# Performance work log

Hardware: AMD Instinct MI355X
Metric: run time of the kernel (lower is better)

Reference implementation:

```python
import jax, jax.numpy as jnp
import numpy as np

G, N, C, R, NCOMP, F = 1, 2097152, 16, 320, 48, 27


def _interp_plane(src, u, v):
    # src: (G, C, H, W). Torch grid_sample convention: u (grid x) indexes W (last dim),
    # v (grid y) indexes H. align_corners=True, bilinear, zero padding. Returns (G, N, C).
    _, _, H, W = src.shape
    x = (u + 1.0) * 0.5 * (W - 1)
    y = (v + 1.0) * 0.5 * (H - 1)
    x0 = jnp.floor(x)
    y0 = jnp.floor(y)
    wx = x - x0
    wy = y - y0
    x0i = x0.astype(jnp.int32)
    y0i = y0.astype(jnp.int32)

    def corner(xi, yi, w):
        inb = ((xi >= 0) & (xi < W) & (yi >= 0) & (yi < H)).astype(src.dtype)
        xc = jnp.clip(xi, 0, W - 1)
        yc = jnp.clip(yi, 0, H - 1)
        vals = jax.vmap(lambda s, yy, xx: s[:, yy, xx])(src, yc, xc)  # (G, C, N)
        return vals * (w * inb)[:, None, :]

    out = (corner(x0i, y0i, (1.0 - wx) * (1.0 - wy))
           + corner(x0i + 1, y0i, wx * (1.0 - wy))
           + corner(x0i, y0i + 1, (1.0 - wx) * wy)
           + corner(x0i + 1, y0i + 1, wx * wy))
    return out.transpose(0, 2, 1)  # (G, N, C)


def _interp_line(src, t):
    # src: (G, C, L), t in [-1, 1]. 1D linear interp, align_corners=True, zero padding.
    _, _, L = src.shape
    x = (t + 1.0) * 0.5 * (L - 1)
    x0 = jnp.floor(x)
    wx = x - x0
    x0i = x0.astype(jnp.int32)

    def corner(xi, w):
        inb = ((xi >= 0) & (xi < L)).astype(src.dtype)
        xc = jnp.clip(xi, 0, L - 1)
        vals = jax.vmap(lambda s, xx: s[:, xx])(src, xc)  # (G, C, N)
        return vals * (w * inb)[:, None, :]

    out = corner(x0i, 1.0 - wx) + corner(x0i + 1, wx)
    return out.transpose(0, 2, 1)  # (G, N, C)


def setup_inputs() -> dict:
    key = jax.random.key(0)
    ks = jax.random.split(key, 8)
    return {
        "points": jax.random.uniform(ks[0], (G, N, 3), jnp.float32, minval=-1.0, maxval=1.0),
        "matrix_components_xy": jax.random.normal(ks[1], (G, C, R, R), jnp.float32) * 0.1,
        "matrix_components_yz": jax.random.normal(ks[2], (G, C, R, R), jnp.float32) * 0.1,
        "matrix_components_xz": jax.random.normal(ks[3], (G, C, R, R), jnp.float32) * 0.1,
        "vector_components_x": jax.random.normal(ks[4], (G, C, R), jnp.float32) * 0.1,
        "vector_components_y": jax.random.normal(ks[5], (G, C, R), jnp.float32) * 0.1,
        "vector_components_z": jax.random.normal(ks[6], (G, C, R), jnp.float32) * 0.1,
        "basis_matrix": jax.random.normal(ks[7], (G, NCOMP, F), jnp.float32) * 0.1,
    }


def reference(points, matrix_components_xy, matrix_components_yz, matrix_components_xz,
              vector_components_x, vector_components_y, vector_components_z, basis_matrix):
    recorded_shape = points.shape
    p = points.reshape(points.shape[0], -1, points.shape[-1])  # (G, N, 3)
    px, py, pz = p[..., 0], p[..., 1], p[..., 2]
    # points[..., :2] -> grid x = px (indexes W of xy plane), grid y = py
    a = _interp_plane(matrix_components_xy, px, py) * _interp_line(vector_components_z, pz)
    # points[..., [0, 2]] -> grid x = px, grid y = pz
    b = _interp_plane(matrix_components_xz, px, pz) * _interp_line(vector_components_y, py)
    # points[..., 1:] -> grid x = py, grid y = pz
    c = _interp_plane(matrix_components_yz, py, pz) * _interp_line(vector_components_x, px)
    feats = jnp.concatenate((a, b, c), axis=-1)  # (G, N, 3C)
    result = jnp.einsum('gnc,gcf->gnf', feats, basis_matrix)  # (G, N, F)
    return result.reshape(*recorded_shape[:-1], -1)
```

## Files before the change

kernel.cpp:

```cpp
#include <hip/hip_runtime.h>
#include <hip/hip_fp16.h>
#include <stdint.h>


constexpr int NPTS = 2097152;
constexpr int CCH  = 16;
constexpr int RES  = 320;
constexpr long long HW = (long long)RES * RES;
constexpr int FD   = 27;
constexpr int BLK  = 256;
constexpr int EBLK = 512;
constexpr int CDIM = 16;
constexpr int NCELL = CDIM * CDIM * CDIM;
constexpr int PATCH = 22;
constexpr int PP_U4 = PATCH * PATCH * 2;
constexpr int PL_U4 = 3 * PP_U4;
constexpr int LN_U4 = 3 * PATCH * 2;
constexpr int SORT_BLOCKS = 256;
constexpr int PTS_PER_SORT = NPTS / SORT_BLOCKS;
constexpr int SORT_G = PTS_PER_SORT / (BLK * 4);

constexpr int PLANE_BLOCKS = 1200;
constexpr int LINE_BLOCKS = 4;

constexpr size_t WS_PLANEH = 0;
constexpr size_t WS_LINEH  = WS_PLANEH + 3ull*HW*CCH*2;
constexpr size_t WS_BFRAG  = WS_LINEH + 3ull*RES*CCH*2;
constexpr size_t WS_CHIST  = WS_BFRAG + 3072;
constexpr size_t WS_CURSOR = WS_CHIST + (size_t)NCELL*4;
constexpr size_t WS_SORTED = WS_CURSOR + (size_t)NCELL*4;
constexpr size_t WS_NEED   = WS_SORTED + (size_t)NPTS*16;

typedef _Float16 half8 __attribute__((ext_vector_type(8)));
typedef float f32x16 __attribute__((ext_vector_type(16)));

__device__ __forceinline__ int cell_key16(float px, float py, float pz) {
    int cx = min(max((int)((px + 1.f) * 8.f), 0), 15);
    int cy = min(max((int)((py + 1.f) * 8.f), 0), 15);
    int cz = min(max((int)((pz + 1.f) * 8.f), 0), 15);
    return (cz << 8) | (cy << 4) | cx;
}

__global__ __launch_bounds__(BLK) void prep_kernel(
    const float* __restrict__ pts,
    const float* __restrict__ pxy, const float* __restrict__ pxz, const float* __restrict__ pyz,
    const float* __restrict__ vx, const float* __restrict__ vy, const float* __restrict__ vz,
    const float* __restrict__ basis,
    __half* __restrict__ planesH, __half* __restrict__ linesH, __half* __restrict__ bfragH,
    unsigned* __restrict__ chist) {
    __shared__ unsigned lh[NCELL];
    const int bid = blockIdx.x;
    const int tid = threadIdx.x;
    if (bid < SORT_BLOCKS) {
        #pragma unroll
        for (int k = 0; k < NCELL / BLK; ++k) lh[tid + k * BLK] = 0u;
        __syncthreads();
        const float4* p4 = ((const float4*)pts) + (size_t)bid * (PTS_PER_SORT * 3 / 4);
        #pragma unroll
        for (int g = 0; g < SORT_G; ++g) {
            const int t = g * BLK + tid;
            const float4 a = p4[t*3+0], b = p4[t*3+1], c = p4[t*3+2];
            atomicAdd(&lh[cell_key16(a.x, a.y, a.z)], 1u);
            atomicAdd(&lh[cell_key16(a.w, b.x, b.y)], 1u);
            atomicAdd(&lh[cell_key16(b.z, b.w, c.x)], 1u);
            atomicAdd(&lh[cell_key16(c.y, c.z, c.w)], 1u);
        }
        __syncthreads();
        #pragma unroll
        for (int k = 0; k < NCELL / BLK; ++k) {
            const int i = tid + k * BLK;
            if (lh[i]) atomicAdd(&chist[i], lh[i]);
        }
    } else if (bid < SORT_BLOCKS + PLANE_BLOCKS) {
        const int pb = bid - SORT_BLOCKS;
        const int plane = pb / 400;
        const int texel = (pb % 400) * BLK + tid;
        const float* src = (plane == 0) ? pxy : (plane == 1 ? pxz : pyz);
        union { ushort u[16]; uint4 q[2]; } pk;
        #pragma unroll
        for (int c = 0; c < CCH; ++c)
            pk.u[c] = __half_as_ushort(__float2half(src[(size_t)c * HW + texel]));
        uint4* dst = (uint4*)(planesH + ((size_t)plane * HW + texel) * CCH);
        dst[0] = pk.q[0]; dst[1] = pk.q[1];
    } else if (bid < SORT_BLOCKS + PLANE_BLOCKS + LINE_BLOCKS) {
        const int idx = (bid - SORT_BLOCKS - PLANE_BLOCKS) * BLK + tid;
        if (idx >= 3 * RES) return;
        const int axis = idx / RES, t = idx % RES;
        const float* src = (axis == 0) ? vx : (axis == 1 ? vy : vz);
        union { ushort u[16]; uint4 q[2]; } pk;
        #pragma unroll
        for (int c = 0; c < CCH; ++c)
            pk.u[c] = __half_as_ushort(__float2half(src[c * RES + t]));
        uint4* dst = (uint4*)(linesH + ((size_t)axis * RES + t) * CCH);
        dst[0] = pk.q[0]; dst[1] = pk.q[1];
    } else {
        if (tid < 192) {
            const int r = tid >> 6, l = tid & 63;
            const int col = l & 31, kb = l >> 5;
            __half* dst = bfragH + tid * 8;
            #pragma unroll
            for (int j = 0; j < 8; ++j) {
                float v = (col < FD) ? basis[(r * 16 + kb * 8 + j) * FD + col] : 0.f;
                dst[j] = __float2half(v);
            }
        }
    }
}

__global__ __launch_bounds__(1024) void scan_kernel(const unsigned* __restrict__ chist,
                                                    unsigned* __restrict__ cursor) {
    __shared__ unsigned lsum[1024];
    const int t = threadIdx.x;
    const uint4 v = ((const uint4*)chist)[t];
    const unsigned run = v.x + v.y + v.z + v.w;
    lsum[t] = run;
    __syncthreads();
    for (int o = 1; o < 1024; o <<= 1) {
        unsigned u = (t >= o) ? lsum[t - o] : 0u;
        __syncthreads();
        lsum[t] += u;
        __syncthreads();
    }
    const unsigned b = lsum[t] - run;
    ((uint4*)cursor)[t] = make_uint4(b, b + v.x, b + v.x + v.y, b + v.x + v.y + v.z);
}

__global__ __launch_bounds__(BLK) void scatter_kernel(const float* __restrict__ pts,
                                                      unsigned* __restrict__ cursor,
                                                      float4* __restrict__ sorted) {
    __shared__ unsigned lh[NCELL];
    __shared__ unsigned lh2[NCELL];
    __shared__ unsigned lb[NCELL];
    const int bid = blockIdx.x;
    const int tid = threadIdx.x;
    #pragma unroll
    for (int k = 0; k < NCELL / BLK; ++k) { lh[tid + k*BLK] = 0u; lh2[tid + k*BLK] = 0u; }
    __syncthreads();
    const float4* p4 = ((const float4*)pts) + (size_t)bid * (PTS_PER_SORT * 3 / 4);
    #pragma unroll
    for (int g = 0; g < SORT_G; ++g) {
        const int t = g * BLK + tid;
        const float4 a = p4[t*3+0], b = p4[t*3+1], c = p4[t*3+2];
        atomicAdd(&lh[cell_key16(a.x, a.y, a.z)], 1u);
        atomicAdd(&lh[cell_key16(a.w, b.x, b.y)], 1u);
        atomicAdd(&lh[cell_key16(b.z, b.w, c.x)], 1u);
        atomicAdd(&lh[cell_key16(c.y, c.z, c.w)], 1u);
    }
    __syncthreads();
    #pragma unroll
    for (int k = 0; k < NCELL / BLK; ++k) {
        const int i = tid + k * BLK;
        lb[i] = lh[i] ? atomicAdd(&cursor[i], lh[i]) : 0u;
    }
    __syncthreads();
    const int ibase = bid * PTS_PER_SORT;
    #pragma unroll
    for (int g = 0; g < SORT_G; ++g) {
        const int t = g * BLK + tid;
        const float4 a = p4[t*3+0], b = p4[t*3+1], c = p4[t*3+2];
        const int i0 = ibase + t * 4;
        int k; unsigned r;
        k = cell_key16(a.x, a.y, a.z); r = atomicAdd(&lh2[k], 1u);
        sorted[lb[k] + r] = make_float4(a.x, a.y, a.z, __int_as_float(i0 + 0));
        k = cell_key16(a.w, b.x, b.y); r = atomicAdd(&lh2[k], 1u);
        sorted[lb[k] + r] = make_float4(a.w, b.x, b.y, __int_as_float(i0 + 1));
        k = cell_key16(b.z, b.w, c.x); r = atomicAdd(&lh2[k], 1u);
        sorted[lb[k] + r] = make_float4(b.z, b.w, c.x, __int_as_float(i0 + 2));
        k = cell_key16(c.y, c.z, c.w); r = atomicAdd(&lh2[k], 1u);
        sorted[lb[k] + r] = make_float4(c.y, c.z, c.w, __int_as_float(i0 + 3));
    }
}

__device__ __forceinline__ half8 interp8_lds(const uint4* __restrict__ sp,
                                             int i00, int i01, int i10, int i11,
                                             int il0, int il1,
                                             float wc, float wr, float lw) {
    union U { uint4 u; __half2 h2[4]; half8 v; };
    U c00, c01, c10, c11, la, lb, res;
    c00.u = sp[i00]; c01.u = sp[i01];
    c10.u = sp[i10]; c11.u = sp[i11];
    la.u  = sp[il0]; lb.u  = sp[il1];
    const float w00 = (1.f - wc) * (1.f - wr), w01 = wc * (1.f - wr);
    const float w10 = (1.f - wc) * wr,         w11 = wc * wr;
    const __half2 w00h = __float2half2_rn(w00), w01h = __float2half2_rn(w01);
    const __half2 w10h = __float2half2_rn(w10), w11h = __float2half2_rn(w11);
    const __half2 lwh  = __float2half2_rn(lw),  mlwh = __float2half2_rn(1.f - lw);
    #pragma unroll
    for (int q = 0; q < 4; ++q) {
        __half2 s = __hmul2(c00.h2[q], w00h);
        s = __hfma2(c01.h2[q], w01h, s);
        s = __hfma2(c10.h2[q], w10h, s);
        s = __hfma2(c11.h2[q], w11h, s);
        __half2 l = __hmul2(la.h2[q], mlwh);
        l = __hfma2(lb.h2[q], lwh, l);
        res.h2[q] = __hmul2(s, l);
    }
    return res.v;
}

__global__ __launch_bounds__(EBLK) void eval_kernel(
    const float4* __restrict__ sorted,
    const __half* __restrict__ planesH,
    const __half* __restrict__ linesH,
    const __half* __restrict__ bfragH,
    const unsigned* __restrict__ chist,
    const unsigned* __restrict__ cursor,
    float* __restrict__ out) {
    __shared__ uint4 s_patch[PL_U4 + LN_U4];
    __shared__ int s_oi[EBLK];
    const int bid = blockIdx.x;
    const int tid = threadIdx.x;
    const int cell = (bid & 7) * (NCELL / 8) + (bid >> 3);
    const int cx = cell & 15, cy = (cell >> 4) & 15, cz = cell >> 8;
    const int bx = (cx * 319) >> 4, by = (cy * 319) >> 4, bz = (cz * 319) >> 4;

    for (int i = tid; i < PL_U4; i += EBLK) {
        const int p = i / PP_U4, rem = i - p * PP_U4;
        const int r = rem / 44, c4 = rem - r * 44;
        const int tx = c4 >> 1, h = c4 & 1;
        const int rb = (p == 0) ? by : bz;
        const int cb = (p == 2) ? by : bx;
        const int gr = min(rb + r, RES - 1), gc = min(cb + tx, RES - 1);
        s_patch[i] = ((const uint4*)(planesH + ((size_t)p * HW + (size_t)gr * RES + gc) * CCH))[h];
    }
    for (int i = tid; i < LN_U4; i += EBLK) {
        const int a = i / 44, rem = i - a * 44;
        const int t = rem >> 1, h = rem & 1;
        const int ab = (a == 0) ? bx : (a == 1) ? by : bz;
        const int gt = min(ab + t, RES - 1);
        s_patch[PL_U4 + i] = ((const uint4*)(linesH + ((size_t)a * RES + gt) * CCH))[h];
    }

    const int wid = tid >> 6, lane = tid & 63;
    const int pcol = lane & 31, kb = lane >> 5;
    union BU { uint4 u; half8 h; } b0u, b1u, b2u;
    const uint4* bf = (const uint4*)bfragH;
    b0u.u = bf[lane]; b1u.u = bf[64 + lane]; b2u.u = bf[128 + lane];

    __syncthreads();

    const int cnt = (int)chist[cell];
    const int start = (int)cursor[cell] - cnt;

    for (int base = 0; base < cnt; base += EBLK) {
        const int tb = wid * 64 + ((lane & 32) ? 0 : 0);
        #pragma unroll
        for (int t = 0; t < 2; ++t) {
            const int tile = wid * 64 + t * 32;
            if (base + tile < cnt) {
                const int slot = base + tile + pcol;
                const float4 pt = sorted[start + min(slot, cnt - 1)];
                if (kb == 0) s_oi[tile + pcol] = __float_as_int(pt.w);

                const float scl = 0.5f * (RES - 1);
                const float fx = (pt.x + 1.f) * scl, fy = (pt.y + 1.f) * scl, fz = (pt.z + 1.f) * scl;
                const float xf = floorf(fx), yf = floorf(fy), zf = floorf(fz);
                const float wx = fx - xf, wy = fy - yf, wz = fz - zf;
                int x0 = min(max((int)xf, 0), RES - 1);
                int y0 = min(max((int)yf, 0), RES - 1);
                int z0 = min(max((int)zf, 0), RES - 1);
                const int x1 = min(x0 + 1, RES - 1);
                const int y1 = min(y0 + 1, RES - 1);
                const int z1 = min(z0 + 1, RES - 1);
                const int lx0 = x0 - bx, lx1 = x1 - bx;
                const int ly0 = y0 - by, ly1 = y1 - by;
                const int lz0 = z0 - bz, lz1 = z1 - bz;

                f32x16 acc;
                #pragma unroll
                for (int r = 0; r < 16; ++r) acc[r] = 0.f;

                half8 a0 = interp8_lds(s_patch,
                    (ly0*PATCH + lx0)*2 + kb, (ly0*PATCH + lx1)*2 + kb,
                    (ly1*PATCH + lx0)*2 + kb, (ly1*PATCH + lx1)*2 + kb,
                    PL_U4 + 2*44 + lz0*2 + kb, PL_U4 + 2*44 + lz1*2 + kb, wx, wy, wz);
                acc = __builtin_amdgcn_mfma_f32_32x32x16_f16(a0, b0u.h, acc, 0, 0, 0);
                half8 a1 = interp8_lds(s_patch,
                    PP_U4 + (lz0*PATCH + lx0)*2 + kb, PP_U4 + (lz0*PATCH + lx1)*2 + kb,
                    PP_U4 + (lz1*PATCH + lx0)*2 + kb, PP_U4 + (lz1*PATCH + lx1)*2 + kb,
                    PL_U4 + 1*44 + ly0*2 + kb, PL_U4 + 1*44 + ly1*2 + kb, wx, wz, wy);
                acc = __builtin_amdgcn_mfma_f32_32x32x16_f16(a1, b1u.h, acc, 0, 0, 0);
                half8 a2 = interp8_lds(s_patch,
                    2*PP_U4 + (lz0*PATCH + ly0)*2 + kb, 2*PP_U4 + (lz0*PATCH + ly1)*2 + kb,
                    2*PP_U4 + (lz1*PATCH + ly0)*2 + kb, 2*PP_U4 + (lz1*PATCH + ly1)*2 + kb,
                    PL_U4 + 0*44 + lx0*2 + kb, PL_U4 + 0*44 + lx1*2 + kb, wy, wz, wx);
                acc = __builtin_amdgcn_mfma_f32_32x32x16_f16(a2, b2u.h, acc, 0, 0, 0);

                if (pcol < FD) {
                    #pragma unroll
                    for (int r = 0; r < 16; ++r) {
                        const int row = (r & 3) + 8 * (r >> 2) + 4 * kb;
                        if (base + tile + row < cnt) {
                            const int o = s_oi[tile + row];
                            out[(size_t)o * FD + pcol] = acc[r];
                        }
                    }
                }
            }
        }
    }
}

__device__ __forceinline__ float bilerp(const float* __restrict__ p,
                                        int o00, int o01, int o10, int o11,
                                        float wc, float wr) {
    float v00 = p[o00], v01 = p[o01], v10 = p[o10], v11 = p[o11];
    float top = v00 + wc * (v01 - v00);
    float bot = v10 + wc * (v11 - v10);
    return top + wr * (bot - top);
}

__global__ __launch_bounds__(BLK) void vm_eval_fallback(
    const float* __restrict__ pts,
    const float* __restrict__ pxy, const float* __restrict__ pyz, const float* __restrict__ pxz,
    const float* __restrict__ vx, const float* __restrict__ vy, const float* __restrict__ vz,
    const float* __restrict__ basis, float* __restrict__ out) {
    const long long i = (long long)blockIdx.x * BLK + threadIdx.x;
    const float px = pts[i*3], py = pts[i*3+1], pz = pts[i*3+2];
    const float scl = 0.5f * (RES - 1);
    const float fx = (px + 1.f) * scl, fy = (py + 1.f) * scl, fz = (pz + 1.f) * scl;
    const float xf = floorf(fx), yf = floorf(fy), zf = floorf(fz);
    const float wx = fx - xf, wy = fy - yf, wz = fz - zf;
    int x0 = min(max((int)xf, 0), RES - 1);
    int y0 = min(max((int)yf, 0), RES - 1);
    int z0 = min(max((int)zf, 0), RES - 1);
    const int x1 = min(x0+1, RES-1), y1 = min(y0+1, RES-1), z1 = min(z0+1, RES-1);
    float acc[FD];
    #pragma unroll
    for (int f = 0; f < FD; ++f) acc[f] = 0.f;
    #pragma unroll 4
    for (int c = 0; c < CCH; ++c) {
        const float* a = pxy + c * HW;
        const float* b = pxz + c * HW;
        const float* d = pyz + c * HW;
        float lz = vz[c*RES+z0]; lz += wz * (vz[c*RES+z1] - lz);
        float ly = vy[c*RES+y0]; ly += wy * (vy[c*RES+y1] - ly);
        float lx = vx[c*RES+x0]; lx += wx * (vx[c*RES+x1] - lx);
        const float fa = bilerp(a, y0*RES+x0, y0*RES+x1, y1*RES+x0, y1*RES+x1, wx, wy) * lz;
        const float fb = bilerp(b, z0*RES+x0, z0*RES+x1, z1*RES+x0, z1*RES+x1, wx, wz) * ly;
        const float fc = bilerp(d, z0*RES+y0, z0*RES+y1, z1*RES+y0, z1*RES+y1, wy, wz) * lx;
        #pragma unroll
        for (int f = 0; f < FD; ++f)
            acc[f] += fa * basis[c*FD+f] + fb * basis[(CCH+c)*FD+f] + fc * basis[(2*CCH+c)*FD+f];
    }
    float* op = out + i * FD;
    #pragma unroll
    for (int f = 0; f < FD; ++f) op[f] = acc[f];
}

extern "C" void kernel_launch(void* const* d_in, const int* in_sizes, int n_in,
                              void* d_out, int out_size, void* d_ws, size_t ws_size,
                              hipStream_t stream) {
    const float* pts   = (const float*)d_in[0];
    const float* pxy   = (const float*)d_in[1];
    const float* pyz   = (const float*)d_in[2];
    const float* pxz   = (const float*)d_in[3];
    const float* vx    = (const float*)d_in[4];
    const float* vy    = (const float*)d_in[5];
    const float* vz    = (const float*)d_in[6];
    const float* basis = (const float*)d_in[7];
    float* out = (float*)d_out;

    if (ws_size < WS_NEED) {
        vm_eval_fallback<<<NPTS / BLK, BLK, 0, stream>>>(pts, pxy, pyz, pxz, vx, vy, vz, basis, out);
        return;
    }

    uint8_t* w = (uint8_t*)d_ws;
    __half*   planesH = (__half*)(w + WS_PLANEH);
    __half*   linesH  = (__half*)(w + WS_LINEH);
    __half*   bfragH  = (__half*)(w + WS_BFRAG);
    unsigned* chist   = (unsigned*)(w + WS_CHIST);
    unsigned* cursor  = (unsigned*)(w + WS_CURSOR);
    float4*   sorted  = (float4*)(w + WS_SORTED);

    hipMemsetAsync(chist, 0, (size_t)NCELL * 4, stream);
    prep_kernel<<<SORT_BLOCKS + PLANE_BLOCKS + LINE_BLOCKS + 1, BLK, 0, stream>>>(
        pts, pxy, pxz, pyz, vx, vy, vz, basis, planesH, linesH, bfragH, chist);
    scan_kernel<<<1, 1024, 0, stream>>>(chist, cursor);
    scatter_kernel<<<SORT_BLOCKS, BLK, 0, stream>>>(pts, cursor, sorted);
    eval_kernel<<<NCELL, EBLK, 0, stream>>>(sorted, planesH, linesH, bfragH, chist, cursor, out);
}
```

Measured before the change: 166.6 us.

## Split LDS patch into half-planes and broadcast output indices via shuffles

Changes the shared-memory patch layout from interleaved 16-byte halves per texel to two separate half-planes, so the two k-halves of a wavefront read contiguous texels. The aim is to reduce LDS bank conflicts on the bilinear gather reads. It also drops the shared s_oi index buffer and instead broadcasts each point's output index with cross-lane shuffles before the scattered stores. This removes LDS writes and reads but adds 16 shuffles per tile.

New measurement: 163.8 us. No clear change (-1.7%).

```diff
diff --git a/kernel.cpp b/kernel.cpp
--- a/kernel.cpp
+++ b/kernel.cpp
@@ -13,7 +13,8 @@
 constexpr int CDIM = 16;
 constexpr int NCELL = CDIM * CDIM * CDIM;
 constexpr int PATCH = 22;
-constexpr int PP_U4 = PATCH * PATCH * 2;
+constexpr int PP_HALF = PATCH * PATCH;
+constexpr int PP_U4 = PP_HALF * 2;
 constexpr int PL_U4 = 3 * PP_U4;
 constexpr int LN_U4 = 3 * PATCH * 2;
 constexpr int SORT_BLOCKS = 256;
@@ -207,7 +208,6 @@
     const unsigned* __restrict__ cursor,
     float* __restrict__ out) {
     __shared__ uint4 s_patch[PL_U4 + LN_U4];
-    __shared__ int s_oi[EBLK];
     const int bid = blockIdx.x;
     const int tid = threadIdx.x;
     const int cell = (bid & 7) * (NCELL / 8) + (bid >> 3);
@@ -216,8 +216,8 @@
 
     for (int i = tid; i < PL_U4; i += EBLK) {
         const int p = i / PP_U4, rem = i - p * PP_U4;
-        const int r = rem / 44, c4 = rem - r * 44;
-        const int tx = c4 >> 1, h = c4 & 1;
+        const int h = rem / PP_HALF, t = rem - h * PP_HALF;
+        const int r = t / PATCH, tx = t - r * PATCH;
         const int rb = (p == 0) ? by : bz;
         const int cb = (p == 2) ? by : bx;
         const int gr = min(rb + r, RES - 1), gc = min(cb + tx, RES - 1);
@@ -225,7 +225,7 @@
     }
     for (int i = tid; i < LN_U4; i += EBLK) {
         const int a = i / 44, rem = i - a * 44;
-        const int t = rem >> 1, h = rem & 1;
+        const int h = rem / PATCH, t = rem - h * PATCH;
         const int ab = (a == 0) ? bx : (a == 1) ? by : bz;
         const int gt = min(ab + t, RES - 1);
         s_patch[PL_U4 + i] = ((const uint4*)(linesH + ((size_t)a * RES + gt) * CCH))[h];
@@ -237,20 +237,22 @@
     const uint4* bf = (const uint4*)bfragH;
     b0u.u = bf[lane]; b1u.u = bf[64 + lane]; b2u.u = bf[128 + lane];
 
+    const int khalf = kb * PP_HALF;
+    const int klin  = kb * PATCH;
+
     __syncthreads();
 
     const int cnt = (int)chist[cell];
     const int start = (int)cursor[cell] - cnt;
 
     for (int base = 0; base < cnt; base += EBLK) {
-        const int tb = wid * 64 + ((lane & 32) ? 0 : 0);
         #pragma unroll
         for (int t = 0; t < 2; ++t) {
             const int tile = wid * 64 + t * 32;
             if (base + tile < cnt) {
                 const int slot = base + tile + pcol;
                 const float4 pt = sorted[start + min(slot, cnt - 1)];
-                if (kb == 0) s_oi[tile + pcol] = __float_as_int(pt.w);
+                const int oi = __float_as_int(pt.w);
 
                 const float scl = 0.5f * (RES - 1);
                 const float fx = (pt.x + 1.f) * scl, fy = (pt.y + 1.f) * scl, fz = (pt.z + 1.f) * scl;
@@ -271,28 +273,33 @@
                 for (int r = 0; r < 16; ++r) acc[r] = 0.f;
 
                 half8 a0 = interp8_lds(s_patch,
-                    (ly0*PATCH + lx0)*2 + kb, (ly0*PATCH + lx1)*2 + kb,
-                    (ly1*PATCH + lx0)*2 + kb, (ly1*PATCH + lx1)*2 + kb,
-                    PL_U4 + 2*44 + lz0*2 + kb, PL_U4 + 2*44 + lz1*2 + kb, wx, wy, wz);
+                    khalf + ly0*PATCH + lx0, khalf + ly0*PATCH + lx1,
+                    khalf + ly1*PATCH + lx0, khalf + ly1*PATCH + lx1,
+                    PL_U4 + 2*44 + klin + lz0, PL_U4 + 2*44 + klin + lz1, wx, wy, wz);
                 acc = __builtin_amdgcn_mfma_f32_32x32x16_f16(a0, b0u.h, acc, 0, 0, 0);
                 half8 a1 = interp8_lds(s_patch,
-                    PP_U4 + (lz0*PATCH + lx0)*2 + kb, PP_U4 + (lz0*PATCH + lx1)*2 + kb,
-                    PP_U4 + (lz1*PATCH + lx0)*2 + kb, PP_U4 + (lz1*PATCH + lx1)*2 + kb,
-                    PL_U4 + 1*44 + ly0*2 + kb, PL_U4 + 1*44 + ly1*2 + kb, wx, wz, wy);
+                    PP_U4 + khalf + lz0*PATCH + lx0, PP_U4 + khalf + lz0*PATCH + lx1,
+                    PP_U4 + khalf + lz1*PATCH + lx0, PP_U4 + khalf + lz1*PATCH + lx1,
+                    PL_U4 + 1*44 + klin + ly0, PL_U4 + 1*44 + klin + ly1, wx, wz, wy);
                 acc = __builtin_amdgcn_mfma_f32_32x32x16_f16(a1, b1u.h, acc, 0, 0, 0);
                 half8 a2 = interp8_lds(s_patch,
-                    2*PP_U4 + (lz0*PATCH + ly0)*2 + kb, 2*PP_U4 + (lz0*PATCH + ly1)*2 + kb,
-                    2*PP_U4 + (lz1*PATCH + ly0)*2 + kb, 2*PP_U4 + (lz1*PATCH + ly1)*2 + kb,
-                    PL_U4 + 0*44 + lx0*2 + kb, PL_U4 + 0*44 + lx1*2 + kb, wy, wz, wx);
+                    2*PP_U4 + khalf + lz0*PATCH + ly0, 2*PP_U4 + khalf + lz0*PATCH + ly1,
+                    2*PP_U4 + khalf + lz1*PATCH + ly0, 2*PP_U4 + khalf + lz1*PATCH + ly1,
+                    PL_U4 + 0*44 + klin + lx0, PL_U4 + 0*44 + klin + lx1, wy, wz, wx);
                 acc = __builtin_amdgcn_mfma_f32_32x32x16_f16(a2, b2u.h, acc, 0, 0, 0);
 
+                int orow[16];
+                #pragma unroll
+                for (int r = 0; r < 16; ++r) {
+                    const int row = (r & 3) + 8 * (r >> 2) + 4 * kb;
+                    orow[r] = __shfl(oi, row, 64);
+                }
                 if (pcol < FD) {
                     #pragma unroll
                     for (int r = 0; r < 16; ++r) {
                         const int row = (r & 3) + 8 * (r >> 2) + 4 * kb;
                         if (base + tile + row < cnt) {
-                            const int o = s_oi[tile + row];
-                            out[(size_t)o * FD + pcol] = acc[r];
+                            out[(size_t)orow[r] * FD + pcol] = acc[r];
                         }
                     }
                 }
```
